# Kernel optimization log

Measured on AMD Instinct MI355X. Metric: run time of the kernel, lower is better.

Reference implementation:

```python
import jax, jax.numpy as jnp
from jax import lax
import numpy as np

IOU_THRESHOLD = 0.35
SCORE_THRESHOLD = 0.5


def _pairwise_iou(b):
    # b: [N,4] boxes in (ymin, xmin, ymax, xmax) convention (tf boxes)
    y1, x1, y2, x2 = b[:, 0], b[:, 1], b[:, 2], b[:, 3]
    area = (y2 - y1) * (x2 - x1)
    iy1 = jnp.maximum(y1[:, None], y1[None, :])
    ix1 = jnp.maximum(x1[:, None], x1[None, :])
    iy2 = jnp.minimum(y2[:, None], y2[None, :])
    ix2 = jnp.minimum(x2[:, None], x2[None, :])
    inter = jnp.maximum(iy2 - iy1, 0.0) * jnp.maximum(ix2 - ix1, 0.0)
    union = area[:, None] + area[None, :] - inter
    return jnp.where(union > 0, inter / union, 0.0)  # [N,N]


def _nms_sample_image(scores, boxes, anchors_wh, num_samples):
    # scores [N], boxes [N,4], anchors_wh [N,2]
    N = scores.shape[0]
    order = jnp.argsort(-scores)  # descending by score, like tf NMS
    s = scores[order]
    b = boxes[order]
    a = anchors_wh[order]
    valid = s > SCORE_THRESHOLD
    iou = _pairwise_iou(b)  # [N,N] on score-sorted boxes
    idx = jnp.arange(N)

    # greedy suppression: box i kept iff valid and no earlier kept box overlaps > thr
    def step(keep, i):
        suppressed = jnp.any(keep & (idx < i) & (iou[i] > IOU_THRESHOLD))
        return keep.at[i].set(valid[i] & ~suppressed), None

    keep, _ = lax.scan(step, jnp.zeros(N, dtype=bool), idx)

    # gather kept entries in (descending-score) order, then pad/slice to num_samples
    rank = jnp.cumsum(keep) - 1  # output slot for each kept entry
    slot = jnp.where(keep, jnp.minimum(rank, num_samples), num_samples)
    vals = jnp.concatenate([s[:, None], b, a], axis=1)  # [N,7]
    out = jnp.zeros((num_samples + 1, 7), vals.dtype).at[slot].set(vals)
    return out[:num_samples]  # [num_samples, 7] = (score | box(4) | anchor_wh(2))


def reference(scores, boxes, anchors, num_samples):
    # scores [B,H,W,1], boxes [B,H,W,4], anchors [B,H,W,4] (last 2 chans = w,h)
    B = scores.shape[0]
    sc = scores.reshape(B, -1)
    bx = boxes.reshape(B, -1, 4)
    an = anchors[..., 2:].reshape(B, -1, 2)
    out = jax.vmap(lambda s, b, a: _nms_sample_image(s, b, a, num_samples))(sc, bx, an)
    return out  # [B, num_samples, 7]


def setup_inputs() -> dict:
    key = jax.random.key(0)
    k1, k2, k3, k4, k5 = jax.random.split(key, 5)
    B, H, W = 8, 64, 64
    scores = jax.random.uniform(k1, (B, H, W, 1), dtype=jnp.float32)
    # well-formed tf boxes: ymin<ymax, xmin<xmax in [0,1]
    ymin = jax.random.uniform(k2, (B, H, W, 1), dtype=jnp.float32) * 0.8
    xmin = jax.random.uniform(k3, (B, H, W, 1), dtype=jnp.float32) * 0.8
    hh = jax.random.uniform(k4, (B, H, W, 1), dtype=jnp.float32) * 0.18 + 0.02
    ww = jax.random.uniform(k5, (B, H, W, 1), dtype=jnp.float32) * 0.18 + 0.02
    boxes = jnp.concatenate([ymin, xmin, ymin + hh, xmin + ww], axis=-1)
    # anchors: [cy, cx, w, h]-style; only last two channels are used
    k6 = jax.random.fold_in(key, 6)
    anchors = jax.random.uniform(k6, (B, H, W, 4), dtype=jnp.float32) * 0.25 + 0.05
    return {"scores": scores, "boxes": boxes, "anchors": anchors, "num_samples": 300}
```

## Files before the change

### kernel.cpp

```cpp
#include <hip/hip_runtime.h>

static constexpr float kIouT = 0.35f;
static constexpr float kScoreT = 0.5f;
static constexpr int kMaxNW = 36;
static constexpr int kStrideW = 37;
static constexpr int kDepth = 3;
static constexpr int kProdWaves = 7;
static constexpr int kRowsPW = 10;
static constexpr int kMaxKeep = 512;

__device__ __forceinline__ float iou_f(const float4 a, const float4 b) {
  float areaA = __fmul_rn(a.z - a.x, a.w - a.y);
  float areaB = __fmul_rn(b.z - b.x, b.w - b.y);
  float iy1 = fmaxf(a.x, b.x);
  float ix1 = fmaxf(a.y, b.y);
  float iy2 = fminf(a.z, b.z);
  float ix2 = fminf(a.w, b.w);
  float dy = fmaxf(iy2 - iy1, 0.0f);
  float dx = fmaxf(ix2 - ix1, 0.0f);
  float inter = __fmul_rn(dy, dx);
  float uni = (areaA + areaB) - inter;
  return (uni > 0.0f) ? __fdiv_rn(inter, uni) : 0.0f;
}

__global__ __launch_bounds__(256)
void nms_count_kernel(const float* __restrict__ scores, int* __restrict__ Mcnt,
                      int N) {
  __shared__ int part[4];
  const int img = blockIdx.x, tid = threadIdx.x, lane = tid & 63, wv = tid >> 6;
  const float4* sc4 = (const float4*)(scores + (size_t)img * N);
  int c = 0;
  for (int q = tid; q < (N >> 2); q += 256) {
    float4 v = sc4[q];
    c += (v.x > kScoreT) + (v.y > kScoreT) + (v.z > kScoreT) + (v.w > kScoreT);
  }
#pragma unroll
  for (int off = 1; off < 64; off <<= 1) c += __shfl_xor(c, off, 64);
  if (lane == 0) part[wv] = c;
  __syncthreads();
  if (tid == 0) Mcnt[img] = part[0] + part[1] + part[2] + part[3];
}

__global__ __launch_bounds__(256)
void nms_rank_kernel(const float* __restrict__ scores,
                     const float4* __restrict__ boxes,
                     unsigned long long* __restrict__ skeys,
                     float4* __restrict__ sboxes, int N) {
  const int wid = (int)(((unsigned)blockIdx.x * blockDim.x + threadIdx.x) >> 6);
  const int lane = threadIdx.x & 63;
  const int img = wid / N;
  const int row = wid - img * N;
  const float* sc = scores + (size_t)img * N;
  const float si = sc[row];
  if (!(si > kScoreT)) return;
  const float4* sc4 = (const float4*)sc;
  int cnt = 0;
  for (int q = lane; q < (N >> 2); q += 64) {
    const float4 v = sc4[q];
    const int j = q << 2;
    cnt += (v.x > si) + (v.y > si) + (v.z > si) + (v.w > si);
    if (v.x == si && j < row) cnt++;
    if (v.y == si && j + 1 < row) cnt++;
    if (v.z == si && j + 2 < row) cnt++;
    if (v.w == si && j + 3 < row) cnt++;
  }
#pragma unroll
  for (int off = 1; off < 64; off <<= 1) cnt += __shfl_xor(cnt, off, 64);
  if (lane == 0) {
    skeys[(size_t)img * N + cnt] =
        ((unsigned long long)(~__float_as_uint(si)) << 32) | (unsigned)row;
    sboxes[(size_t)img * N + cnt] = boxes[(size_t)img * N + row];
  }
}

__global__ __launch_bounds__(256)
void nms_mask_kernel(const float4* __restrict__ sboxes,
                     const int* __restrict__ Mcnt,
                     unsigned long long* __restrict__ mask,
                     int N, int totalRows) {
  const int wid = (int)(((unsigned)blockIdx.x * blockDim.x + threadIdx.x) >> 6);
  const int lane = threadIdx.x & 63;
  if (wid >= totalRows) return;
  const int img = wid / N;
  const int row = wid - img * N;
  const int m = Mcnt[img];
  if (row >= m) return;
  const float4* sb = sboxes + (size_t)img * N;
  const float4 bi = sb[row];
  const int nw = (m + 63) >> 6;
  unsigned long long* mrow = mask + (size_t)wid * (size_t)(N >> 6);
  for (int w = row >> 6; w < nw; ++w) {
    int j = (w << 6) | lane;
    bool sup = false;
    if (j > row && j < m) sup = iou_f(bi, sb[j]) > kIouT;
    unsigned long long bm = __ballot(sup);
    if (lane == 0) mrow[w] = bm;
  }
}

__global__ __launch_bounds__(512)
void nms_scan_kernel(const unsigned long long* __restrict__ skeys,
                     const float4* __restrict__ sboxes,
                     const int* __restrict__ Mcnt,
                     const unsigned long long* __restrict__ mask,
                     const float* __restrict__ anchors,
                     float* __restrict__ out, int N, int NS) {
  __shared__ unsigned long long lbuf[kDepth * 64 * kStrideW];
  __shared__ int keptlist[kMaxKeep];
  __shared__ int s_done, s_kept;
  const int img = blockIdx.x;
  const int tid = threadIdx.x;
  const int lane = tid & 63;
  const int wv = tid >> 6;
  const int m = Mcnt[img];
  const int nw = (m + 63) >> 6;
  const int stride = N >> 6;
  const unsigned long long* mbase = mask + (size_t)img * (size_t)N * stride;
  const unsigned long long* kg = skeys + (size_t)img * N;
  const float4* sb = sboxes + (size_t)img * N;
  const float* an = anchors + (size_t)img * (size_t)N * 4;
  float* o = out + (size_t)img * NS * 7;
  if (tid == 0) { s_done = 0; s_kept = 0; }

  int kept = 0;
  unsigned long long remv = 0ull;

  if (m > 0 && nw <= kMaxNW) {
    const int pw = wv - 1;
    unsigned long long pv[kRowsPW];
    auto issue = [&](int cc) {
      if (cc >= nw) return;
      const int base = cc << 6;
      const int rlim = min(m - base, 64);
      const int w = cc + lane;
      const bool wok = (w < nw);
#pragma unroll
      for (int k = 0; k < kRowsPW; ++k) {
        const int r = pw + k * kProdWaves;
        if (r < rlim && wok) pv[k] = mbase[(size_t)(base + r) * stride + w];
      }
    };
    auto commit = [&](int cc) {
      if (cc >= nw) return;
      const int base = cc << 6;
      const int rlim = min(m - base, 64);
      const int w = cc + lane;
      const bool wok = (w < nw);
      unsigned long long* dst = lbuf + (size_t)(cc % kDepth) * 64 * kStrideW;
#pragma unroll
      for (int k = 0; k < kRowsPW; ++k) {
        const int r = pw + k * kProdWaves;
        if (r < rlim && wok) dst[(size_t)r * kStrideW + w] = pv[k];
      }
    };
    if (wv != 0) {
      issue(0); commit(0);
      issue(1);
    }
    __syncthreads();
    for (int c = 0; c < nw; ++c) {
      if (wv == 0) {
        const unsigned long long* buf = lbuf + (size_t)(c % kDepth) * 64 * kStrideW;
        const unsigned long long diag = buf[(size_t)lane * kStrideW + c];
        unsigned long long local = __shfl(remv, c, 64);
        const int rem = m - (c << 6);
        unsigned long long avail = ~local;
        if (rem < 64) avail &= ((1ull << rem) - 1ull);
        while (avail != 0ull && kept < NS) {
          const int b = __builtin_ctzll(avail);
          if (lane == 0) keptlist[kept] = (c << 6) + b;
          kept++;
          const unsigned long long rc = __shfl(diag, b, 64);
          if (lane > c && lane < nw)
            remv |= buf[(size_t)b * kStrideW + lane];
          local |= rc;
          avail &= ~local;
          avail &= ~(1ull << b);
        }
        if (lane == 0 && kept >= NS) s_done = 1;
      } else {
        commit(c + 1);
        issue(c + 2);
      }
      __syncthreads();
      if (s_done) break;
    }
  } else if (m > 0) {
    if (wv == 0) {
      for (int i = 0; i < m && kept < NS; ++i) {
        const unsigned long long rw = __shfl(remv, i >> 6, 64);
        if ((rw >> (i & 63)) & 1ull) continue;
        if (lane == 0) keptlist[kept] = i;
        kept++;
        const unsigned long long* mrow = mbase + (size_t)i * stride;
        if (lane >= (i >> 6) && lane < nw) remv |= mrow[lane];
      }
    }
  }

  if (wv == 0 && lane == 0) s_kept = kept;
  __syncthreads();
  const int K = s_kept;
  for (int t = tid; t < K; t += 512) {
    const int i = keptlist[t];
    const unsigned long long ki = kg[i];
    const float4 bi = sb[i];
    const unsigned idx = (unsigned)ki;
    float* row = o + t * 7;
    row[0] = __uint_as_float(~(unsigned)(ki >> 32));
    row[1] = bi.x; row[2] = bi.y; row[3] = bi.z; row[4] = bi.w;
    row[5] = an[idx * 4 + 2];
    row[6] = an[idx * 4 + 3];
  }
  for (int t = K * 7 + tid; t < NS * 7; t += 512) o[t] = 0.0f;
}

__global__ __launch_bounds__(1024)
void nms_fused_kernel(const float* __restrict__ scores,
                      const float4* __restrict__ boxes,
                      const float* __restrict__ anchors,
                      float* __restrict__ out, int N, int NS) {
  __shared__ unsigned long long keys[4096];
  __shared__ int s_m;
  if (N > 4096) return;
  const int img = blockIdx.x;
  const int tid = threadIdx.x;
  const float* sc = scores + (size_t)img * N;
  const float4* bx = boxes + (size_t)img * N;
  if (tid == 0) s_m = 0;
  __syncthreads();
  int cnt = 0;
  for (int i = tid; i < N; i += blockDim.x) {
    float s = sc[i];
    keys[i] = ((unsigned long long)(~__float_as_uint(s)) << 32) | (unsigned)i;
    if (s > kScoreT) cnt++;
  }
  if (cnt) atomicAdd(&s_m, cnt);
  __syncthreads();
  for (int k = 2; k <= N; k <<= 1) {
    for (int j = k >> 1; j > 0; j >>= 1) {
      for (int i = tid; i < N; i += blockDim.x) {
        int ixj = i ^ j;
        if (ixj > i) {
          unsigned long long a = keys[i];
          unsigned long long b = keys[ixj];
          bool up = ((i & k) == 0);
          if (up ? (a > b) : (a < b)) { keys[i] = b; keys[ixj] = a; }
        }
      }
      __syncthreads();
    }
  }
  if (tid >= 64) return;
  const int lane = tid;
  const int m = s_m;
  const int nw = (m + 63) >> 6;
  const float* an = anchors + (size_t)img * N * 4;
  float* o = out + (size_t)img * NS * 7;
  unsigned long long remv = 0ull;
  int kept = 0;
  for (int i = 0; i < m && kept < NS; ++i) {
    unsigned long long rw = __shfl(remv, i >> 6, 64);
    if ((rw >> (i & 63)) & 1ull) continue;
    unsigned long long ki = keys[i];
    float4 bi = bx[(unsigned)ki];
    if (lane == 0) {
      unsigned idx = (unsigned)ki;
      float* row = o + kept * 7;
      row[0] = __uint_as_float(~(unsigned)(ki >> 32));
      row[1] = bi.x; row[2] = bi.y; row[3] = bi.z; row[4] = bi.w;
      row[5] = an[idx * 4 + 2];
      row[6] = an[idx * 4 + 3];
    }
    kept++;
    for (int w2 = i >> 6; w2 < nw; ++w2) {
      int j = (w2 << 6) | lane;
      bool sup = false;
      if (j > i && j < m) sup = iou_f(bi, bx[(unsigned)keys[j]]) > kIouT;
      unsigned long long bm = __ballot(sup);
      if (lane == w2) remv |= bm;
    }
  }
  for (int t = kept * 7 + lane; t < NS * 7; t += 64) o[t] = 0.0f;
}

extern "C" void kernel_launch(void* const* d_in, const int* in_sizes, int n_in,
                              void* d_out, int out_size, void* d_ws, size_t ws_size,
                              hipStream_t stream) {
  const float* scores = (const float*)d_in[0];
  const float4* boxes = (const float4*)d_in[1];
  const float* anchors = (const float*)d_in[2];
  float* out = (float*)d_out;
  const int B = 8;
  const int N = in_sizes[0] / B;
  const int NS = out_size / (B * 7);

  const size_t nTot = (size_t)B * (size_t)N;
  const size_t keysB = nTot * 8;
  const size_t sboxB = nTot * 16;
  const size_t mcntB = 256;
  const size_t maskB = nTot * (size_t)(N >> 6) * 8;
  const size_t need = keysB + sboxB + mcntB + maskB;

  if (ws_size >= need && (N % 256) == 0 && N >= 256 && NS <= kMaxKeep) {
    char* p = (char*)d_ws;
    unsigned long long* skeys = (unsigned long long*)p; p += keysB;
    float4* sboxes = (float4*)p;                         p += sboxB;
    int* Mcnt = (int*)p;                                 p += mcntB;
    unsigned long long* mask = (unsigned long long*)p;

    nms_count_kernel<<<B, 256, 0, stream>>>(scores, Mcnt, N);
    const int totalRows = B * N;
    const int rankBlocks = (int)(((long long)totalRows * 64 + 255) / 256);
    nms_rank_kernel<<<rankBlocks, 256, 0, stream>>>(scores, boxes, skeys,
                                                    sboxes, N);
    nms_mask_kernel<<<rankBlocks, 256, 0, stream>>>(sboxes, Mcnt, mask, N,
                                                    totalRows);
    nms_scan_kernel<<<B, 512, 0, stream>>>(skeys, sboxes, Mcnt, mask, anchors,
                                           out, N, NS);
  } else {
    nms_fused_kernel<<<B, 1024, 0, stream>>>(scores, boxes, anchors, out, N, NS);
  }
}
```

Measured before the change: 114.1 us.

## Fuse count into rank kernel, stage scores/boxes in LDS, batch scan row merges

Folds the score-count kernel into the rank kernel as extra blocks, which removes one launch. The rank and mask kernels move to 1024-thread blocks that stage each image's scores or sorted boxes in shared memory, so every row no longer re-reads them from global memory. The scan kernel now stores the diagonal words in their own buffer and uses readlane in place of shuffles. It also defers the OR of kept-row masks until after the serial in-chunk loop, which shortens the critical path. The larger shared buffers limit N to at most 4096 and may reduce occupancy.

```diff
diff --git a/kernel.cpp b/kernel.cpp
--- a/kernel.cpp
+++ b/kernel.cpp
@@ -2,8 +2,8 @@
 
 static constexpr float kIouT = 0.35f;
 static constexpr float kScoreT = 0.5f;
-static constexpr int kMaxNW = 36;
-static constexpr int kStrideW = 37;
+static constexpr int kMaxNW = 40;
+static constexpr int kStrideW = 40;
 static constexpr int kDepth = 3;
 static constexpr int kProdWaves = 7;
 static constexpr int kRowsPW = 10;
@@ -23,78 +23,109 @@
   return (uni > 0.0f) ? __fdiv_rn(inter, uni) : 0.0f;
 }
 
-__global__ __launch_bounds__(256)
-void nms_count_kernel(const float* __restrict__ scores, int* __restrict__ Mcnt,
-                      int N) {
-  __shared__ int part[4];
-  const int img = blockIdx.x, tid = threadIdx.x, lane = tid & 63, wv = tid >> 6;
-  const float4* sc4 = (const float4*)(scores + (size_t)img * N);
-  int c = 0;
-  for (int q = tid; q < (N >> 2); q += 256) {
-    float4 v = sc4[q];
-    c += (v.x > kScoreT) + (v.y > kScoreT) + (v.z > kScoreT) + (v.w > kScoreT);
-  }
-#pragma unroll
-  for (int off = 1; off < 64; off <<= 1) c += __shfl_xor(c, off, 64);
-  if (lane == 0) part[wv] = c;
-  __syncthreads();
-  if (tid == 0) Mcnt[img] = part[0] + part[1] + part[2] + part[3];
-}
-
-__global__ __launch_bounds__(256)
+__device__ __forceinline__ unsigned long long rdlane64(unsigned long long v,
+                                                       int l) {
+  unsigned lo = (unsigned)__builtin_amdgcn_readlane((int)(unsigned)v, l);
+  unsigned hi = (unsigned)__builtin_amdgcn_readlane((int)(unsigned)(v >> 32), l);
+  return ((unsigned long long)hi << 32) | lo;
+}
+
+__global__ __launch_bounds__(1024)
 void nms_rank_kernel(const float* __restrict__ scores,
                      const float4* __restrict__ boxes,
                      unsigned long long* __restrict__ skeys,
-                     float4* __restrict__ sboxes, int N) {
-  const int wid = (int)(((unsigned)blockIdx.x * blockDim.x + threadIdx.x) >> 6);
-  const int lane = threadIdx.x & 63;
-  const int img = wid / N;
-  const int row = wid - img * N;
+                     float4* __restrict__ sboxes,
+                     int* __restrict__ Mcnt, int N, int rankBlocks) {
+  const int tid = threadIdx.x;
+  const int lane = tid & 63;
+  const int wv = tid >> 6;
+  if ((int)blockIdx.x >= rankBlocks) {
+    __shared__ int part[16];
+    const int img = blockIdx.x - rankBlocks;
+    const float4* sc4 = (const float4*)(scores + (size_t)img * N);
+    int c = 0;
+    for (int q = tid; q < (N >> 2); q += 1024) {
+      float4 v = sc4[q];
+      c += (v.x > kScoreT) + (v.y > kScoreT) + (v.z > kScoreT) + (v.w > kScoreT);
+    }
+#pragma unroll
+    for (int off = 1; off < 64; off <<= 1) c += __shfl_xor(c, off, 64);
+    if (lane == 0) part[wv] = c;
+    __syncthreads();
+    if (tid == 0) {
+      int s = 0;
+      for (int k = 0; k < 16; ++k) s += part[k];
+      Mcnt[img] = s;
+    }
+    return;
+  }
+  __shared__ __align__(16) float ssc[4096];
+  const int wpb = N >> 6;
+  const int img = blockIdx.x / wpb;
+  const int rowbase = (blockIdx.x - img * wpb) << 6;
   const float* sc = scores + (size_t)img * N;
-  const float si = sc[row];
-  if (!(si > kScoreT)) return;
-  const float4* sc4 = (const float4*)sc;
-  int cnt = 0;
-  for (int q = lane; q < (N >> 2); q += 64) {
-    const float4 v = sc4[q];
-    const int j = q << 2;
-    cnt += (v.x > si) + (v.y > si) + (v.z > si) + (v.w > si);
-    if (v.x == si && j < row) cnt++;
-    if (v.y == si && j + 1 < row) cnt++;
-    if (v.z == si && j + 2 < row) cnt++;
-    if (v.w == si && j + 3 < row) cnt++;
-  }
-#pragma unroll
-  for (int off = 1; off < 64; off <<= 1) cnt += __shfl_xor(cnt, off, 64);
-  if (lane == 0) {
-    skeys[(size_t)img * N + cnt] =
-        ((unsigned long long)(~__float_as_uint(si)) << 32) | (unsigned)row;
-    sboxes[(size_t)img * N + cnt] = boxes[(size_t)img * N + row];
-  }
-}
-
-__global__ __launch_bounds__(256)
+  for (int q = tid; q < N; q += 1024) ssc[q] = sc[q];
+  __syncthreads();
+  const float4* s4 = (const float4*)ssc;
+#pragma unroll
+  for (int rr = 0; rr < 4; ++rr) {
+    const int row = rowbase + (wv << 2) + rr;
+    const float si = ssc[row];
+    if (!(si > kScoreT)) continue;
+    int cnt = 0;
+    for (int q = lane; q < (N >> 2); q += 64) {
+      const float4 v = s4[q];
+      const int j = q << 2;
+      cnt += (v.x > si) + (v.y > si) + (v.z > si) + (v.w > si);
+      if (v.x == si && j < row) cnt++;
+      if (v.y == si && j + 1 < row) cnt++;
+      if (v.z == si && j + 2 < row) cnt++;
+      if (v.w == si && j + 3 < row) cnt++;
+    }
+#pragma unroll
+    for (int off = 1; off < 64; off <<= 1) cnt += __shfl_xor(cnt, off, 64);
+    if (lane == 0) {
+      skeys[(size_t)img * N + cnt] =
+          ((unsigned long long)(~__float_as_uint(si)) << 32) | (unsigned)row;
+      sboxes[(size_t)img * N + cnt] = boxes[(size_t)img * N + row];
+    }
+  }
+}
+
+__global__ __launch_bounds__(1024)
 void nms_mask_kernel(const float4* __restrict__ sboxes,
                      const int* __restrict__ Mcnt,
-                     unsigned long long* __restrict__ mask,
-                     int N, int totalRows) {
-  const int wid = (int)(((unsigned)blockIdx.x * blockDim.x + threadIdx.x) >> 6);
-  const int lane = threadIdx.x & 63;
-  if (wid >= totalRows) return;
-  const int img = wid / N;
-  const int row = wid - img * N;
+                     unsigned long long* __restrict__ mask, int N) {
+  __shared__ float4 ssb[4096];
+  const int tid = threadIdx.x;
+  const int lane = tid & 63;
+  const int wv = tid >> 6;
+  const int wpb = N >> 6;
+  const int img = blockIdx.x / wpb;
+  const int rowbase = (blockIdx.x - img * wpb) << 6;
   const int m = Mcnt[img];
-  if (row >= m) return;
-  const float4* sb = sboxes + (size_t)img * N;
-  const float4 bi = sb[row];
+  if (rowbase >= m) return;
+  const int cnt = m - rowbase;
   const int nw = (m + 63) >> 6;
-  unsigned long long* mrow = mask + (size_t)wid * (size_t)(N >> 6);
-  for (int w = row >> 6; w < nw; ++w) {
-    int j = (w << 6) | lane;
-    bool sup = false;
-    if (j > row && j < m) sup = iou_f(bi, sb[j]) > kIouT;
-    unsigned long long bm = __ballot(sup);
-    if (lane == 0) mrow[w] = bm;
+  const int wb = rowbase >> 6;
+  const int stride = N >> 6;
+  const float4* sb = sboxes + (size_t)img * N + rowbase;
+  for (int q = tid; q < cnt; q += 1024) ssb[q] = sb[q];
+  __syncthreads();
+#pragma unroll
+  for (int rr = 0; rr < 4; ++rr) {
+    const int rl = (wv << 2) + rr;
+    if (rl >= cnt) continue;
+    const float4 bi = ssb[rl];
+    unsigned long long* mrow =
+        mask + (size_t)(img * N + rowbase + rl) * stride;
+    for (int w = wb; w < nw; ++w) {
+      const int jl = ((w - wb) << 6) | lane;
+      bool sup = false;
+      if (jl > rl && jl < cnt) sup = iou_f(bi, ssb[jl]) > kIouT;
+      const unsigned long long bm = __ballot(sup);
+      if (lane == 0) mrow[w] = bm;
+    }
   }
 }
 
@@ -105,14 +136,16 @@
                      const unsigned long long* __restrict__ mask,
                      const float* __restrict__ anchors,
                      float* __restrict__ out, int N, int NS) {
-  __shared__ unsigned long long lbuf[kDepth * 64 * kStrideW];
+  __shared__ unsigned long long lbuf[kDepth][64][kStrideW];
+  __shared__ unsigned long long dbuf[kDepth][64];
   __shared__ int keptlist[kMaxKeep];
   __shared__ int s_done, s_kept;
   const int img = blockIdx.x;
   const int tid = threadIdx.x;
   const int lane = tid & 63;
   const int wv = tid >> 6;
-  const int m = Mcnt[img];
+  int m = Mcnt[img];
+  if (m > N) m = N;
   const int nw = (m + 63) >> 6;
   const int stride = N >> 6;
   const unsigned long long* mbase = mask + (size_t)img * (size_t)N * stride;
@@ -146,36 +179,46 @@
       const int rlim = min(m - base, 64);
       const int w = cc + lane;
       const bool wok = (w < nw);
-      unsigned long long* dst = lbuf + (size_t)(cc % kDepth) * 64 * kStrideW;
+      const int bufi = cc % kDepth;
 #pragma unroll
       for (int k = 0; k < kRowsPW; ++k) {
         const int r = pw + k * kProdWaves;
-        if (r < rlim && wok) dst[(size_t)r * kStrideW + w] = pv[k];
+        if (r < rlim && wok) {
+          lbuf[bufi][r][w - cc] = pv[k];
+          if (lane == 0) dbuf[bufi][r] = pv[k];
+        }
       }
     };
-    if (wv != 0) {
-      issue(0); commit(0);
-      issue(1);
-    }
+    if (wv != 0) { issue(0); commit(0); issue(1); }
     __syncthreads();
     for (int c = 0; c < nw; ++c) {
       if (wv == 0) {
-        const unsigned long long* buf = lbuf + (size_t)(c % kDepth) * 64 * kStrideW;
-        const unsigned long long diag = buf[(size_t)lane * kStrideW + c];
-        unsigned long long local = __shfl(remv, c, 64);
-        const int rem = m - (c << 6);
+        const int bufi = c % kDepth;
+        const int cb = c << 6;
+        const unsigned long long diag = dbuf[bufi][lane];
+        unsigned long long local = rdlane64(remv, c);
+        const int rem = m - cb;
         unsigned long long avail = ~local;
-        if (rem < 64) avail &= ((1ull << rem) - 1ull);
+        if (rem < 64) avail &= (1ull << rem) - 1ull;
+        unsigned long long keptbits = 0ull;
         while (avail != 0ull && kept < NS) {
-          const int b = __builtin_ctzll(avail);
-          if (lane == 0) keptlist[kept] = (c << 6) + b;
+          const int b = (int)__builtin_ctzll(avail);
+          if (lane == 0) keptlist[kept] = cb + b;
           kept++;
-          const unsigned long long rc = __shfl(diag, b, 64);
-          if (lane > c && lane < nw)
-            remv |= buf[(size_t)b * kStrideW + lane];
+          keptbits |= 1ull << b;
+          const unsigned long long rc = rdlane64(diag, b);
           local |= rc;
           avail &= ~local;
           avail &= ~(1ull << b);
+        }
+        const bool lok = (lane > c) && (lane < nw);
+        const int widx = lok ? (lane - c) : 0;
+        unsigned long long kb = keptbits;
+        while (kb != 0ull) {
+          const int b = (int)__builtin_ctzll(kb);
+          kb &= kb - 1ull;
+          const unsigned long long t = lbuf[bufi][b][widx];
+          if (lok) remv |= t;
         }
         if (lane == 0 && kept >= NS) s_done = 1;
       } else {
@@ -183,12 +226,12 @@
         issue(c + 2);
       }
       __syncthreads();
-      if (s_done) break;
+      if (s_done != 0) break;
     }
   } else if (m > 0) {
     if (wv == 0) {
       for (int i = 0; i < m && kept < NS; ++i) {
-        const unsigned long long rw = __shfl(remv, i >> 6, 64);
+        const unsigned long long rw = rdlane64(remv, i >> 6);
         if ((rw >> (i & 63)) & 1ull) continue;
         if (lane == 0) keptlist[kept] = i;
         kept++;
@@ -302,20 +345,19 @@
   const size_t maskB = nTot * (size_t)(N >> 6) * 8;
   const size_t need = keysB + sboxB + mcntB + maskB;
 
-  if (ws_size >= need && (N % 256) == 0 && N >= 256 && NS <= kMaxKeep) {
+  if (ws_size >= need && (N % 256) == 0 && N >= 256 && N <= 4096 &&
+      NS <= kMaxKeep) {
     char* p = (char*)d_ws;
     unsigned long long* skeys = (unsigned long long*)p; p += keysB;
     float4* sboxes = (float4*)p;                         p += sboxB;
     int* Mcnt = (int*)p;                                 p += mcntB;
     unsigned long long* mask = (unsigned long long*)p;
 
-    nms_count_kernel<<<B, 256, 0, stream>>>(scores, Mcnt, N);
-    const int totalRows = B * N;
-    const int rankBlocks = (int)(((long long)totalRows * 64 + 255) / 256);
-    nms_rank_kernel<<<rankBlocks, 256, 0, stream>>>(scores, boxes, skeys,
-                                                    sboxes, N);
-    nms_mask_kernel<<<rankBlocks, 256, 0, stream>>>(sboxes, Mcnt, mask, N,
-                                                    totalRows);
+    const int rankBlocks = B * (N >> 6);
+    nms_rank_kernel<<<rankBlocks + B, 1024, 0, stream>>>(scores, boxes, skeys,
+                                                         sboxes, Mcnt, N,
+                                                         rankBlocks);
+    nms_mask_kernel<<<rankBlocks, 1024, 0, stream>>>(sboxes, Mcnt, mask, N);
     nms_scan_kernel<<<B, 512, 0, stream>>>(skeys, sboxes, Mcnt, mask, anchors,
                                            out, N, NS);
   } else {
```

Result: slower. 151.5 us (+32.8%).
